# Performance work log

Hardware: AMD Instinct MI355X
Metric: run time of the kernel (lower is better)

Reference implementation:

```python
import jax, jax.numpy as jnp
import numpy as np
import math

D_MODEL = 1024
MAX_SEQ_LEN = 2048
BATCH = 4
SEQ_LEN = 2048

def setup_inputs() -> dict:
    key = jax.random.key(0)
    kx, kq, kk, kv = jax.random.split(key, 4)
    x = jax.random.normal(kx, (BATCH, SEQ_LEN, D_MODEL), dtype=jnp.float32)
    # nn.Linear(d_model, d_model, bias=False): weight shape [out, in]; y = x @ W.T
    s = 1.0 / math.sqrt(D_MODEL)
    wq = jax.random.uniform(kq, (D_MODEL, D_MODEL), dtype=jnp.float32, minval=-s, maxval=s)
    wk = jax.random.uniform(kk, (D_MODEL, D_MODEL), dtype=jnp.float32, minval=-s, maxval=s)
    wv = jax.random.uniform(kv, (D_MODEL, D_MODEL), dtype=jnp.float32, minval=-s, maxval=s)
    return {"x": x, "wq": wq, "wk": wk, "wv": wv}

def reference(x, wq, wk, wv):
    # q,k,v: [B, S, D]
    q = jnp.einsum('bsd,ed->bse', x, wq)
    k = jnp.einsum('bsd,ed->bse', x, wk)
    v = jnp.einsum('bsd,ed->bse', x, wv)
    scale = 1.0 / math.sqrt(q.shape[-1])
    scores = jnp.einsum('bqd,bkd->bqk', q, k) * scale  # [B, S, S]
    seq_len = x.shape[1]
    causal = jnp.tril(jnp.ones((seq_len, seq_len), dtype=bool))
    scores = jnp.where(causal[None, :, :], scores, -jnp.inf)
    attn = jax.nn.softmax(scores, axis=-1)
    return jnp.einsum('bqk,bkd->bqd', attn, v)
```

## Files before the change

### kernel.cpp

```cpp
#include <hip/hip_runtime.h>
#include <hip/hip_bf16.h>

typedef unsigned short u16;
typedef __attribute__((ext_vector_type(8))) short short8;
typedef __attribute__((ext_vector_type(4))) float f32x4;

__device__ __forceinline__ u16 f2bf(float f){
  unsigned int u = __builtin_bit_cast(unsigned int, f);
  u += 0x7FFFu + ((u >> 16) & 1u);
  return (u16)(u >> 16);
}
__device__ __forceinline__ float bf2f(u16 b){
  unsigned int u = ((unsigned int)b) << 16;
  return __builtin_bit_cast(float, u);
}

__device__ __forceinline__ void gload_lds16(const u16* g, u16* lds){
  __builtin_amdgcn_global_load_lds(
      (const __attribute__((address_space(1))) unsigned int*)g,
      (__attribute__((address_space(3))) unsigned int*)lds,
      16, 0, 0);
}

template<int MODE>
__launch_bounds__(256, 2)
__global__ void gemm_bt(const u16* __restrict__ A, int lda,
                        const u16* __restrict__ B, int ldb,
                        void* __restrict__ Cout, int ldc,
                        int kIterFixed,
                        long long strideAz, long long strideBz, long long strideCz,
                        float* __restrict__ lsum, float scale)
{
  __shared__ __align__(16) u16 As[2][128*32];
  __shared__ __align__(16) u16 Bs[2][128*32];
  const int bi = blockIdx.x, bj = blockIdx.y, bz = blockIdx.z;
  if (MODE == 1 && bj > bi) return;
  A += (long long)bz * strideAz;
  B += (long long)bz * strideBz;
  const int m0 = bi*128, n0 = bj*128;
  const int kIters = (MODE == 2) ? (bi + 1) * 4 : kIterFixed;
  const int t = threadIdx.x;
  const int lane = t & 63;
  const int w = t >> 6;
  const int wm = w >> 1, wn = w & 1;
  const int la = lane & 15, lb = lane >> 4;

  const int c0 = t,        r0 = c0 >> 2, q0c = (c0 & 3) << 3;
  const int c1 = t + 256,  r1 = c1 >> 2, q1c = (c1 & 3) << 3;
  const int ldsb0 = (t & ~63) << 3;
  const int ldsb1 = (256 + (t & ~63)) << 3;

  f32x4 acc[4][4];
  #pragma unroll
  for (int i = 0; i < 4; i++)
    #pragma unroll
    for (int j = 0; j < 4; j++) acc[i][j] = (f32x4){0.f, 0.f, 0.f, 0.f};

  gload_lds16(A + (long long)(m0 + r0)*lda + q0c, &As[0][ldsb0]);
  gload_lds16(A + (long long)(m0 + r1)*lda + q1c, &As[0][ldsb1]);
  gload_lds16(B + (long long)(n0 + r0)*ldb + q0c, &Bs[0][ldsb0]);
  gload_lds16(B + (long long)(n0 + r1)*ldb + q1c, &Bs[0][ldsb1]);
  asm volatile("s_waitcnt vmcnt(0)" ::: "memory");
  __syncthreads();

  for (int kt = 0; kt < kIters; ++kt){
    const int cur = kt & 1;
    if (kt + 1 < kIters){
      const int k0 = (kt + 1) * 32;
      gload_lds16(A + (long long)(m0 + r0)*lda + k0 + q0c, &As[cur^1][ldsb0]);
      gload_lds16(A + (long long)(m0 + r1)*lda + k0 + q1c, &As[cur^1][ldsb1]);
      gload_lds16(B + (long long)(n0 + r0)*ldb + k0 + q0c, &Bs[cur^1][ldsb0]);
      gload_lds16(B + (long long)(n0 + r1)*ldb + k0 + q1c, &Bs[cur^1][ldsb1]);
    }
    short8 af[4], bfr[4];
    #pragma unroll
    for (int mi = 0; mi < 4; mi++)
      af[mi] = *(const short8*)&As[cur][(wm*64 + mi*16 + la)*32 + lb*8];
    #pragma unroll
    for (int ni = 0; ni < 4; ni++)
      bfr[ni] = *(const short8*)&Bs[cur][(wn*64 + ni*16 + la)*32 + lb*8];
    #pragma unroll
    for (int mi = 0; mi < 4; mi++)
      #pragma unroll
      for (int ni = 0; ni < 4; ni++)
        acc[mi][ni] = __builtin_amdgcn_mfma_f32_16x16x32_bf16(af[mi], bfr[ni], acc[mi][ni], 0, 0, 0);
    asm volatile("s_waitcnt vmcnt(0)" ::: "memory");
    __syncthreads();
  }

  if (MODE == 0){
    u16* C = (u16*)Cout;
    #pragma unroll
    for (int mi = 0; mi < 4; mi++)
      #pragma unroll
      for (int r = 0; r < 4; r++){
        const int row = m0 + wm*64 + mi*16 + lb*4 + r;
        #pragma unroll
        for (int ni = 0; ni < 4; ni++){
          const int col = n0 + wn*64 + ni*16 + la;
          C[(long long)row*ldc + col] = f2bf(acc[mi][ni][r]);
        }
      }
  } else if (MODE == 1){
    u16* C = (u16*)Cout + (long long)bz * strideCz;
    float* lrow = lsum + bz*2048;
    #pragma unroll
    for (int mi = 0; mi < 4; mi++)
      #pragma unroll
      for (int r = 0; r < 4; r++){
        const int row = m0 + wm*64 + mi*16 + lb*4 + r;
        float partial = 0.f;
        #pragma unroll
        for (int ni = 0; ni < 4; ni++){
          const int col = n0 + wn*64 + ni*16 + la;
          float p = 0.f;
          if (col <= row) p = __expf(acc[mi][ni][r] * scale);
          const u16 ub = f2bf(p);
          C[(long long)row*ldc + col] = ub;
          partial += bf2f(ub);
        }
        #pragma unroll
        for (int off = 1; off < 16; off <<= 1) partial += __shfl_xor(partial, off);
        if (la == 0) atomicAdd(&lrow[row], partial);
      }
  } else {
    float* C = (float*)Cout + (long long)bz * strideCz;
    const float* lrow = lsum + bz*2048;
    #pragma unroll
    for (int mi = 0; mi < 4; mi++)
      #pragma unroll
      for (int r = 0; r < 4; r++){
        const int row = m0 + wm*64 + mi*16 + lb*4 + r;
        const float inv = 1.f / lrow[row];
        #pragma unroll
        for (int ni = 0; ni < 4; ni++){
          const int col = n0 + wn*64 + ni*16 + la;
          C[(long long)row*ldc + col] = acc[mi][ni][r] * inv;
        }
      }
  }
}

__global__ void convert_bf16(const float* __restrict__ src, u16* __restrict__ dst, int n4){
  const int i = blockIdx.x*256 + threadIdx.x;
  if (i >= n4) return;
  const float4 v = ((const float4*)src)[i];
  union { u16 u[4]; unsigned long long ll; } o;
  o.u[0] = f2bf(v.x); o.u[1] = f2bf(v.y); o.u[2] = f2bf(v.z); o.u[3] = f2bf(v.w);
  ((unsigned long long*)dst)[i] = o.ll;
}

__global__ void transpose_v(const u16* __restrict__ qkvb, u16* __restrict__ vt){
  __shared__ u16 tile[32][33];
  const int b = blockIdx.z;
  const int s0 = blockIdx.x*32, d0 = blockIdx.y*32;
  const int tx = threadIdx.x, ty = threadIdx.y;
  const u16* src = qkvb + (long long)b*2048*3072 + 2048;
  #pragma unroll
  for (int i = 0; i < 4; i++){
    const int s = ty + i*8;
    tile[s][tx] = src[(long long)(s0 + s)*3072 + d0 + tx];
  }
  __syncthreads();
  u16* dst = vt + (long long)b*1024*2048;
  #pragma unroll
  for (int i = 0; i < 4; i++){
    const int d = ty + i*8;
    dst[(long long)(d0 + d)*2048 + s0 + tx] = tile[tx][d];
  }
}

extern "C" void kernel_launch(void* const* d_in, const int* in_sizes, int n_in,
                              void* d_out, int out_size, void* d_ws, size_t ws_size,
                              hipStream_t stream)
{
  const float* x  = (const float*)d_in[0];
  const float* wq = (const float*)d_in[1];
  const float* wk = (const float*)d_in[2];
  const float* wv = (const float*)d_in[3];

  u16* xb   = (u16*)d_ws;
  u16* wb   = xb   + (size_t)8192*1024;
  u16* qkvb = wb   + (size_t)3072*1024;
  u16* vt   = qkvb + (size_t)8192*3072;
  u16* Pb   = vt   + (size_t)4*1024*2048;
  float* lsum = (float*)(Pb + (size_t)4*2048*2048);

  convert_bf16<<<8192, 256, 0, stream>>>(x,  xb, 2097152);
  convert_bf16<<<1024, 256, 0, stream>>>(wq, wb,                    262144);
  convert_bf16<<<1024, 256, 0, stream>>>(wk, wb + (size_t)1024*1024, 262144);
  convert_bf16<<<1024, 256, 0, stream>>>(wv, wb + (size_t)2048*1024, 262144);

  gemm_bt<0><<<dim3(64, 24, 1), 256, 0, stream>>>(
      xb, 1024, wb, 1024, (void*)qkvb, 3072, 32, 0, 0, 0, nullptr, 1.f);

  transpose_v<<<dim3(64, 32, 4), dim3(32, 8, 1), 0, stream>>>(qkvb, vt);

  hipMemsetAsync(lsum, 0, (size_t)4*2048*sizeof(float), stream);

  gemm_bt<1><<<dim3(16, 16, 4), 256, 0, stream>>>(
      qkvb, 3072, qkvb + 1024, 3072, (void*)Pb, 2048, 32,
      (long long)2048*3072, (long long)2048*3072, (long long)2048*2048,
      lsum, 0.03125f);

  gemm_bt<2><<<dim3(16, 8, 4), 256, 0, stream>>>(
      Pb, 2048, vt, 2048, d_out, 1024, 0,
      (long long)2048*2048, (long long)1024*2048, (long long)2048*1024,
      lsum, 1.f);
}
```

Measured before the change: 263.9 us.

## Move GEMMs to 256x256 tiles with 4-stage swizzled LDS pipeline

Replaces the 128x128, 256-thread double-buffered GEMM with a 256x256, 512-thread kernel. It uses a 4-deep LDS ring buffer with prefetch two stages ahead and an XOR-swizzled LDS layout to avoid bank conflicts. The MFMA work is split into two half-steps separated by barriers, with s_setprio raised around the MFMA bursts, and the projection GEMM gets a grouped block-index swizzle for L2 reuse. The larger tiles cut global traffic per FLOP, but they shrink the grid sharply for the causal attention GEMMs. That risks poor CU utilisation and load imbalance, and the 128KB of LDS limits each CU to one block.

```diff
diff --git a/kernel.cpp b/kernel.cpp
--- a/kernel.cpp
+++ b/kernel.cpp
@@ -14,107 +14,151 @@
   unsigned int u = ((unsigned int)b) << 16;
   return __builtin_bit_cast(float, u);
 }
-
 __device__ __forceinline__ void gload_lds16(const u16* g, u16* lds){
   __builtin_amdgcn_global_load_lds(
       (const __attribute__((address_space(1))) unsigned int*)g,
-      (__attribute__((address_space(3))) unsigned int*)lds,
-      16, 0, 0);
-}
+      (__attribute__((address_space(3))) unsigned int*)lds, 16, 0, 0);
+}
+
+#define FENCE_LGKM0() do { asm volatile("s_waitcnt lgkmcnt(0)" ::: "memory"); \
+                           __builtin_amdgcn_sched_barrier(0); } while(0)
+#define FENCE_VM4()   do { asm volatile("s_waitcnt vmcnt(4)"   ::: "memory"); \
+                           __builtin_amdgcn_sched_barrier(0); } while(0)
 
 template<int MODE>
-__launch_bounds__(256, 2)
-__global__ void gemm_bt(const u16* __restrict__ A, int lda,
+__launch_bounds__(512, 2)
+__global__ void gemm256(const u16* __restrict__ A, int lda,
                         const u16* __restrict__ B, int ldb,
                         void* __restrict__ Cout, int ldc,
-                        int kIterFixed,
+                        int ntFixed,
                         long long strideAz, long long strideBz, long long strideCz,
                         float* __restrict__ lsum, float scale)
 {
-  __shared__ __align__(16) u16 As[2][128*32];
-  __shared__ __align__(16) u16 Bs[2][128*32];
-  const int bi = blockIdx.x, bj = blockIdx.y, bz = blockIdx.z;
-  if (MODE == 1 && bj > bi) return;
+  __shared__ __align__(16) u16 As[4*8192];
+  __shared__ __align__(16) u16 Bs[4*8192];
+
+  int bi, bj;
+  const int bz = blockIdx.z;
+  if (MODE == 0){
+    const int bid = blockIdx.x;
+    const int swz = (bid & 7)*48 + (bid >> 3);
+    bi = swz & 31; bj = swz >> 5;
+  } else {
+    bi = blockIdx.x; bj = blockIdx.y;
+    if (MODE == 1 && bj > bi) return;
+  }
   A += (long long)bz * strideAz;
   B += (long long)bz * strideBz;
-  const int m0 = bi*128, n0 = bj*128;
-  const int kIters = (MODE == 2) ? (bi + 1) * 4 : kIterFixed;
+  const int m0 = bi*256, n0 = bj*256;
+  const int nt = (MODE == 2) ? (bi + 1)*8 : ntFixed;
+
   const int t = threadIdx.x;
   const int lane = t & 63;
   const int w = t >> 6;
-  const int wm = w >> 1, wn = w & 1;
+  const int wm = w >> 2, wn = w & 3;
   const int la = lane & 15, lb = lane >> 4;
 
-  const int c0 = t,        r0 = c0 >> 2, q0c = (c0 & 3) << 3;
-  const int c1 = t + 256,  r1 = c1 >> 2, q1c = (c1 & 3) << 3;
-  const int ldsb0 = (t & ~63) << 3;
-  const int ldsb1 = (256 + (t & ~63)) << 3;
-
-  f32x4 acc[4][4];
-  #pragma unroll
-  for (int i = 0; i < 4; i++)
-    #pragma unroll
-    for (int j = 0; j < 4; j++) acc[i][j] = (f32x4){0.f, 0.f, 0.f, 0.f};
-
-  gload_lds16(A + (long long)(m0 + r0)*lda + q0c, &As[0][ldsb0]);
-  gload_lds16(A + (long long)(m0 + r1)*lda + q1c, &As[0][ldsb1]);
-  gload_lds16(B + (long long)(n0 + r0)*ldb + q0c, &Bs[0][ldsb0]);
-  gload_lds16(B + (long long)(n0 + r1)*ldb + q1c, &Bs[0][ldsb1]);
-  asm volatile("s_waitcnt vmcnt(0)" ::: "memory");
-  __syncthreads();
-
-  for (int kt = 0; kt < kIters; ++kt){
-    const int cur = kt & 1;
-    if (kt + 1 < kIters){
-      const int k0 = (kt + 1) * 32;
-      gload_lds16(A + (long long)(m0 + r0)*lda + k0 + q0c, &As[cur^1][ldsb0]);
-      gload_lds16(A + (long long)(m0 + r1)*lda + k0 + q1c, &As[cur^1][ldsb1]);
-      gload_lds16(B + (long long)(n0 + r0)*ldb + k0 + q0c, &Bs[cur^1][ldsb0]);
-      gload_lds16(B + (long long)(n0 + r1)*ldb + k0 + q1c, &Bs[cur^1][ldsb1]);
+  const int sR0 = w*16 + (lane >> 2);
+  const int sR1 = 128 + sR0;
+  const int scw = ((lane & 3) ^ ((lane >> 2) & 3)) * 8;
+  const u16* gA0 = A + (long long)(m0 + sR0)*lda + scw;
+  const u16* gA1 = A + (long long)(m0 + sR1)*lda + scw;
+  const u16* gB0 = B + (long long)(n0 + sR0)*ldb + scw;
+  const u16* gB1 = B + (long long)(n0 + sR1)*ldb + scw;
+  const int ldsW0 = w*512;
+  const int ldsW1 = 4096 + w*512;
+
+  const int swz4 = (lb ^ (la & 3)) * 8;
+  int rdA[8], rdB[4];
+  #pragma unroll
+  for (int m = 0; m < 8; ++m) rdA[m] = (wm*128 + m*16 + la)*32 + swz4;
+  #pragma unroll
+  for (int n = 0; n < 4; ++n) rdB[n] = (wn*64 + n*16 + la)*32 + swz4;
+
+  f32x4 acc[8][4];
+  #pragma unroll
+  for (int m = 0; m < 8; ++m)
+    #pragma unroll
+    for (int n = 0; n < 4; ++n) acc[m][n] = (f32x4){0.f,0.f,0.f,0.f};
+
+  gload_lds16(gA0,      &As[ldsW0]);        gload_lds16(gA1,      &As[ldsW1]);
+  gload_lds16(gB0,      &Bs[ldsW0]);        gload_lds16(gB1,      &Bs[ldsW1]);
+  gload_lds16(gA0 + 32, &As[8192 + ldsW0]); gload_lds16(gA1 + 32, &As[8192 + ldsW1]);
+  gload_lds16(gB0 + 32, &Bs[8192 + ldsW0]); gload_lds16(gB1 + 32, &Bs[8192 + ldsW1]);
+  FENCE_VM4();
+  __builtin_amdgcn_s_barrier();
+
+  for (int tt = 0; tt < nt; ++tt){
+    const int bb = (tt & 3) * 8192;
+    const int sn = tt + 2;
+    const int sb = (sn & 3) * 8192;
+    short8 af[4], bf[4];
+
+    #pragma unroll
+    for (int m = 0; m < 4; ++m) af[m] = *(const short8*)&As[bb + rdA[m]];
+    #pragma unroll
+    for (int n = 0; n < 4; ++n) bf[n] = *(const short8*)&Bs[bb + rdB[n]];
+    if (sn < nt){
+      gload_lds16(gA0 + sn*32, &As[sb + ldsW0]);
+      gload_lds16(gA1 + sn*32, &As[sb + ldsW1]);
     }
-    short8 af[4], bfr[4];
-    #pragma unroll
-    for (int mi = 0; mi < 4; mi++)
-      af[mi] = *(const short8*)&As[cur][(wm*64 + mi*16 + la)*32 + lb*8];
-    #pragma unroll
-    for (int ni = 0; ni < 4; ni++)
-      bfr[ni] = *(const short8*)&Bs[cur][(wn*64 + ni*16 + la)*32 + lb*8];
-    #pragma unroll
-    for (int mi = 0; mi < 4; mi++)
-      #pragma unroll
-      for (int ni = 0; ni < 4; ni++)
-        acc[mi][ni] = __builtin_amdgcn_mfma_f32_16x16x32_bf16(af[mi], bfr[ni], acc[mi][ni], 0, 0, 0);
-    asm volatile("s_waitcnt vmcnt(0)" ::: "memory");
-    __syncthreads();
+    __builtin_amdgcn_s_barrier();
+    FENCE_LGKM0();
+    __builtin_amdgcn_s_setprio(1);
+    #pragma unroll
+    for (int m = 0; m < 4; ++m)
+      #pragma unroll
+      for (int n = 0; n < 4; ++n)
+        acc[m][n] = __builtin_amdgcn_mfma_f32_16x16x32_bf16(af[m], bf[n], acc[m][n], 0,0,0);
+    __builtin_amdgcn_s_setprio(0);
+    __builtin_amdgcn_s_barrier();
+
+    #pragma unroll
+    for (int m = 0; m < 4; ++m) af[m] = *(const short8*)&As[bb + rdA[4+m]];
+    if (sn < nt){
+      gload_lds16(gB0 + sn*32, &Bs[sb + ldsW0]);
+      gload_lds16(gB1 + sn*32, &Bs[sb + ldsW1]);
+    }
+    __builtin_amdgcn_s_barrier();
+    FENCE_LGKM0();
+    __builtin_amdgcn_s_setprio(1);
+    #pragma unroll
+    for (int m = 0; m < 4; ++m)
+      #pragma unroll
+      for (int n = 0; n < 4; ++n)
+        acc[4+m][n] = __builtin_amdgcn_mfma_f32_16x16x32_bf16(af[m], bf[n], acc[4+m][n], 0,0,0);
+    __builtin_amdgcn_s_setprio(0);
+    FENCE_VM4();
+    __builtin_amdgcn_s_barrier();
   }
 
   if (MODE == 0){
     u16* C = (u16*)Cout;
     #pragma unroll
-    for (int mi = 0; mi < 4; mi++)
-      #pragma unroll
-      for (int r = 0; r < 4; r++){
-        const int row = m0 + wm*64 + mi*16 + lb*4 + r;
-        #pragma unroll
-        for (int ni = 0; ni < 4; ni++){
-          const int col = n0 + wn*64 + ni*16 + la;
-          C[(long long)row*ldc + col] = f2bf(acc[mi][ni][r]);
+    for (int m = 0; m < 8; ++m)
+      #pragma unroll
+      for (int r = 0; r < 4; ++r){
+        const int row = m0 + wm*128 + m*16 + lb*4 + r;
+        #pragma unroll
+        for (int n = 0; n < 4; ++n){
+          const int col = n0 + wn*64 + n*16 + la;
+          C[(long long)row*ldc + col] = f2bf(acc[m][n][r]);
         }
       }
   } else if (MODE == 1){
     u16* C = (u16*)Cout + (long long)bz * strideCz;
     float* lrow = lsum + bz*2048;
     #pragma unroll
-    for (int mi = 0; mi < 4; mi++)
-      #pragma unroll
-      for (int r = 0; r < 4; r++){
-        const int row = m0 + wm*64 + mi*16 + lb*4 + r;
+    for (int m = 0; m < 8; ++m)
+      #pragma unroll
+      for (int r = 0; r < 4; ++r){
+        const int row = m0 + wm*128 + m*16 + lb*4 + r;
         float partial = 0.f;
         #pragma unroll
-        for (int ni = 0; ni < 4; ni++){
-          const int col = n0 + wn*64 + ni*16 + la;
+        for (int n = 0; n < 4; ++n){
+          const int col = n0 + wn*64 + n*16 + la;
           float p = 0.f;
-          if (col <= row) p = __expf(acc[mi][ni][r] * scale);
+          if (col <= row) p = __expf(acc[m][n][r] * scale);
           const u16 ub = f2bf(p);
           C[(long long)row*ldc + col] = ub;
           partial += bf2f(ub);
@@ -127,15 +171,15 @@
     float* C = (float*)Cout + (long long)bz * strideCz;
     const float* lrow = lsum + bz*2048;
     #pragma unroll
-    for (int mi = 0; mi < 4; mi++)
-      #pragma unroll
-      for (int r = 0; r < 4; r++){
-        const int row = m0 + wm*64 + mi*16 + lb*4 + r;
+    for (int m = 0; m < 8; ++m)
+      #pragma unroll
+      for (int r = 0; r < 4; ++r){
+        const int row = m0 + wm*128 + m*16 + lb*4 + r;
         const float inv = 1.f / lrow[row];
         #pragma unroll
-        for (int ni = 0; ni < 4; ni++){
-          const int col = n0 + wn*64 + ni*16 + la;
-          C[(long long)row*ldc + col] = acc[mi][ni][r] * inv;
+        for (int n = 0; n < 4; ++n){
+          const int col = n0 + wn*64 + n*16 + la;
+          C[(long long)row*ldc + col] = acc[m][n][r] * inv;
         }
       }
   }
@@ -187,23 +231,23 @@
   float* lsum = (float*)(Pb + (size_t)4*2048*2048);
 
   convert_bf16<<<8192, 256, 0, stream>>>(x,  xb, 2097152);
-  convert_bf16<<<1024, 256, 0, stream>>>(wq, wb,                    262144);
+  convert_bf16<<<1024, 256, 0, stream>>>(wq, wb,                     262144);
   convert_bf16<<<1024, 256, 0, stream>>>(wk, wb + (size_t)1024*1024, 262144);
   convert_bf16<<<1024, 256, 0, stream>>>(wv, wb + (size_t)2048*1024, 262144);
 
-  gemm_bt<0><<<dim3(64, 24, 1), 256, 0, stream>>>(
+  gemm256<0><<<dim3(384, 1, 1), 512, 0, stream>>>(
       xb, 1024, wb, 1024, (void*)qkvb, 3072, 32, 0, 0, 0, nullptr, 1.f);
 
   transpose_v<<<dim3(64, 32, 4), dim3(32, 8, 1), 0, stream>>>(qkvb, vt);
 
   hipMemsetAsync(lsum, 0, (size_t)4*2048*sizeof(float), stream);
 
-  gemm_bt<1><<<dim3(16, 16, 4), 256, 0, stream>>>(
+  gemm256<1><<<dim3(8, 8, 4), 512, 0, stream>>>(
       qkvb, 3072, qkvb + 1024, 3072, (void*)Pb, 2048, 32,
       (long long)2048*3072, (long long)2048*3072, (long long)2048*2048,
       lsum, 0.03125f);
 
-  gemm_bt<2><<<dim3(16, 8, 4), 256, 0, stream>>>(
+  gemm256<2><<<dim3(8, 4, 4), 512, 0, stream>>>(
       Pb, 2048, vt, 2048, d_out, 1024, 0,
       (long long)2048*2048, (long long)1024*2048, (long long)2048*1024,
       lsum, 1.f);
```

Result: slower. 289.6 us (+9.7%).
